# Kernel optimization log

Measured on AMD Instinct MI355X. Metric: run time of the kernel, lower is better.

Reference implementation:

```python
import jax, jax.numpy as jnp
import numpy as np
from jax import lax

N, C, RC, H, W = 2, 256, 32, 64, 64  # RC = C // 8


def conv1x1(x, w, b):
    # x: [n,c,h,w], w: [o,c], b: [o]
    return jnp.einsum('nchw,oc->nohw', x, w) + b[None, :, None, None]


def conv3x3(x, w, b):
    # x: [n,c,h,w], w: [o,i,3,3]
    y = lax.conv_general_dilated(x, w, window_strides=(1, 1), padding='SAME',
                                 dimension_numbers=('NCHW', 'OIHW', 'NCHW'))
    return y + b[None, :, None, None]


def setup_inputs() -> dict:
    key = jax.random.key(0)
    ks = jax.random.split(key, 16)
    p = lambda k, s: jax.random.normal(k, s, dtype=jnp.float32) * 0.02
    z = lambda o: jnp.zeros((o,), jnp.float32)
    return {
        'rgb_feat': jax.random.normal(ks[0], (N, C, H, W), jnp.float32),
        'chm_feat': jax.random.normal(ks[1], (N, C, H, W), jnp.float32),
        'rgb_q_w': p(ks[2], (RC, C)), 'rgb_q_b': z(RC),
        'rgb_k_w': p(ks[3], (RC, C)), 'rgb_k_b': z(RC),
        'rgb_v_w': p(ks[4], (C, C)), 'rgb_v_b': z(C),
        'depth_q_w': p(ks[5], (RC, C)), 'depth_q_b': z(RC),
        'depth_k_w': p(ks[6], (RC, C)), 'depth_k_b': z(RC),
        'depth_v_w': p(ks[7], (C, C)), 'depth_v_b': z(C),
        'gate_w': p(ks[8], (C, 2 * C)), 'gate_b': z(C),
        'fus1_w': p(ks[9], (2 * C, 2 * C)), 'fus1_b': z(2 * C),
        'fus2_w': p(ks[10], (2 * C, 2 * C, 3, 3)), 'fus2_b': z(2 * C),
        'fus3_w': p(ks[11], (C, 2 * C)), 'fus3_b': z(C),
        'skip_w': p(ks[12], (C, 2 * C)), 'skip_b': z(C),
    }


def reference(rgb_feat, chm_feat,
              rgb_q_w, rgb_q_b, rgb_k_w, rgb_k_b, rgb_v_w, rgb_v_b,
              depth_q_w, depth_q_b, depth_k_w, depth_k_b, depth_v_w, depth_v_b,
              gate_w, gate_b, fus1_w, fus1_b, fus2_w, fus2_b,
              fus3_w, fus3_b, skip_w, skip_b):
    n, c, h, w = rgb_feat.shape
    hw = h * w
    flat = lambda t: t.reshape(n, t.shape[1], hw)

    rq = flat(conv1x1(rgb_feat, rgb_q_w, rgb_q_b))       # [n,rc,hw]
    rk = flat(conv1x1(rgb_feat, rgb_k_w, rgb_k_b))       # [n,rc,hw]
    rv = flat(conv1x1(rgb_feat, rgb_v_w, rgb_v_b))       # [n,c,hw]
    dq = flat(conv1x1(chm_feat, depth_q_w, depth_q_b))   # [n,rc,hw]
    dk = flat(conv1x1(chm_feat, depth_k_w, depth_k_b))   # [n,rc,hw]
    dv = flat(conv1x1(chm_feat, depth_v_w, depth_v_b))   # [n,c,hw]

    # rgb branch attended with depth-derived attention
    rgb_attn = jax.nn.softmax(jnp.einsum('nri,nrj->nij', dq, dk), axis=-1)  # [n,hw,hw]
    br = jnp.einsum('nci,nij->ncj', rv, rgb_attn).reshape(rgb_feat.shape) + rgb_feat

    # depth branch attended with rgb-derived attention
    depth_attn = jax.nn.softmax(jnp.einsum('nri,nrj->nij', rq, rk), axis=-1)
    bd = jnp.einsum('nci,nij->ncj', dv, depth_attn).reshape(chm_feat.shape) + chm_feat

    cat = jnp.concatenate([br, bd], axis=1)              # [n,2c,h,w]
    g = jax.nn.sigmoid(conv1x1(cat, gate_w, gate_b))     # [n,c,h,w]
    c_fused = br * g + bd * (1.0 - g)
    d_fused = br * bd
    f = jnp.concatenate([c_fused, d_fused], axis=1)      # [n,2c,h,w]

    y = jax.nn.relu(conv1x1(f, fus1_w, fus1_b))
    y = jax.nn.relu(conv3x3(y, fus2_w, fus2_b))
    y = conv1x1(y, fus3_w, fus3_b)
    fused = y + conv1x1(f, skip_w, skip_b)
    return fused
```

## Files before the change

kernel.cpp:

```cpp
#include <hip/hip_runtime.h>
#include <stdint.h>


typedef __bf16 bf16_t;
typedef __bf16 bf16x8 __attribute__((ext_vector_type(8)));
typedef float f32x4 __attribute__((ext_vector_type(4)));

#define HW 4096
#define NB 2

__device__ inline f32x4 mfma_bf16(bf16x8 a, bf16x8 b, f32x4 c) {
    return __builtin_amdgcn_mfma_f32_16x16x32_bf16(a, b, c, 0, 0, 0);
}

#define MAXJOB 12
struct CvtJobs {
    const float* src[MAXJOB];
    bf16_t* dst[MAXJOB];
    int vend[MAXJOB];
    int rowlen[MAXJOB];
    int rowstride[MAXJOB];
    int rowoff[MAXJOB];
};

__global__ __launch_bounds__(256) void convert_batch_k(CvtJobs J, int totalvec) {
    int gv = blockIdx.x * 256 + threadIdx.x;
    if (gv >= totalvec) return;
    int j = 0;
    while (gv >= J.vend[j]) j++;
    int vbase = (j == 0) ? 0 : J.vend[j - 1];
    int e = (gv - vbase) * 8;
    const float* s = J.src[j] + e;
    float4 f0 = *(const float4*)s;
    float4 f1 = *(const float4*)(s + 4);
    bf16x8 o;
    o[0] = (bf16_t)f0.x; o[1] = (bf16_t)f0.y; o[2] = (bf16_t)f0.z; o[3] = (bf16_t)f0.w;
    o[4] = (bf16_t)f1.x; o[5] = (bf16_t)f1.y; o[6] = (bf16_t)f1.z; o[7] = (bf16_t)f1.w;
    int di = e;
    if (J.rowlen[j])
        di = (e / J.rowlen[j]) * J.rowstride[j] + J.rowoff[j] + (e % J.rowlen[j]);
    *(bf16x8*)(J.dst[j] + di) = o;
}

__global__ __launch_bounds__(256) void pack_bias_k(const float* qr, const float* kr,
                                                   const float* qd, const float* kd,
                                                   const float* sb, const float* fb,
                                                   float* BQK_R, float* BQK_D, float* BSUM) {
    int t = threadIdx.x;
    if (t < 32) {
        BQK_R[t] = qr[t]; BQK_R[32 + t] = kr[t];
        BQK_D[t] = qd[t]; BQK_D[32 + t] = kd[t];
    }
    BSUM[t] = sb[t] + fb[t];
}

__global__ __launch_bounds__(256) void reorder_fus2_k(const float* __restrict__ src,
                                                      bf16_t* __restrict__ dst) {
    int idx = blockIdx.x * 256 + threadIdx.x;
    if (idx >= 512 * 4608) return;
    int o = idx / 4608;
    int t = idx % 4608;
    int t9 = t / 512;
    int c  = t % 512;
    dst[idx] = (bf16_t)src[(size_t)o * 4608 + c * 9 + t9];
}

template <int EPI, bool OUT_BF16>
__global__ __launch_bounds__(256) void gemm_k(const bf16_t* __restrict__ A,
                                              const bf16_t* __restrict__ A2,
                                              const bf16_t* __restrict__ B,
                                              const float* __restrict__ bias,
                                              const float* __restrict__ bias2,
                                              void* __restrict__ outp,
                                              const void* __restrict__ aux,
                                              int M, int K, size_t strideB, size_t strideO) {
    __shared__ bf16_t Bt[64][72];
    const int t = threadIdx.x;
    const int mb = blockIdx.x, jb = blockIdx.y, n = blockIdx.z;
    const int w = t >> 6, lane = t & 63, quad = lane >> 4, l16 = lane & 15;

    const bf16_t* Au = (n >= 2) ? A2 : A;
    const float* biasu = (n >= 2) ? bias2 : bias;

    const bf16_t* Bb = B + (size_t)n * strideB + jb * 64;
    const int srow = t >> 2;
    const int scol = (t & 3) << 4;

    f32x4 zero = {0.f, 0.f, 0.f, 0.f};
    f32x4 acc[4] = {zero, zero, zero, zero};

    const bf16_t* Arow = Au + (size_t)(mb * 64 + w * 16 + l16) * K + quad * 8;

    for (int k0 = 0; k0 < K; k0 += 64) {
        const bf16_t* src = Bb + (size_t)(k0 + srow) * HW + scol;
        bf16x8 v0 = *(const bf16x8*)src;
        bf16x8 v1 = *(const bf16x8*)(src + 8);
        __syncthreads();
#pragma unroll
        for (int e = 0; e < 8; e++) Bt[scol + e][srow] = v0[e];
#pragma unroll
        for (int e = 0; e < 8; e++) Bt[scol + 8 + e][srow] = v1[e];
        __syncthreads();

        bf16x8 a0 = *(const bf16x8*)(Arow + k0);
        bf16x8 a1 = *(const bf16x8*)(Arow + k0 + 32);
#pragma unroll
        for (int ns = 0; ns < 4; ns++) {
            bf16x8 b0 = *(const bf16x8*)&Bt[ns * 16 + l16][quad * 8];
            bf16x8 b1 = *(const bf16x8*)&Bt[ns * 16 + l16][32 + quad * 8];
            acc[ns] = mfma_bf16(a0, b0, acc[ns]);
            acc[ns] = mfma_bf16(a1, b1, acc[ns]);
        }
    }

    if (EPI == 6) {
#pragma unroll
        for (int ns = 0; ns < 4; ns++) {
            int col = jb * 64 + ns * 16 + l16;
            union { bf16_t h[4]; unsigned long long u; } pk;
#pragma unroll
            for (int rr = 0; rr < 4; rr++) {
                int m = w * 16 + quad * 4 + rr;
                pk.h[rr] = (bf16_t)(acc[ns][rr] + biasu[m]);
            }
            *(unsigned long long*)((bf16_t*)outp +
                ((size_t)n * HW + col) * 64 + w * 16 + quad * 4) = pk.u;
        }
    } else if (EPI == 7) {
        const int m_base = mb * 64 + w * 16 + quad * 4;
#pragma unroll
        for (int ns = 0; ns < 4; ns++) {
            int col = jb * 64 + ns * 16 + l16;
            union { bf16_t h[4]; unsigned long long u; } pk;
#pragma unroll
            for (int rr = 0; rr < 4; rr++) {
                float v = acc[ns][rr] + biasu[m_base + rr];
                pk.h[rr] = (bf16_t)(v > 0.f ? v : 0.f);
            }
            *(unsigned long long*)((bf16_t*)outp +
                ((size_t)n * HW + col) * 512 + m_base) = pk.u;
        }
    } else if (EPI == 5) {
        const bf16_t* catp = (const bf16_t*)aux;
        bf16_t* f = (bf16_t*)outp;
#pragma unroll
        for (int ns = 0; ns < 4; ns++) {
#pragma unroll
            for (int rr = 0; rr < 4; rr++) {
                int m = mb * 64 + w * 16 + quad * 4 + rr;
                int col = jb * 64 + ns * 16 + l16;
                float v = acc[ns][rr] + biasu[m];
                float g = 1.f / (1.f + __expf(-v));
                size_t base = (size_t)n * 512 * HW + (size_t)m * HW + col;
                float br = (float)catp[base];
                float bd = (float)catp[base + (size_t)256 * HW];
                size_t ob = (size_t)n * 1024 * HW + (size_t)m * HW + col;
                f[ob] = (bf16_t)(br * g + bd * (1.f - g));
                f[ob + (size_t)256 * HW] = (bf16_t)(br * bd);
            }
        }
    } else {
#pragma unroll
        for (int ns = 0; ns < 4; ns++) {
#pragma unroll
            for (int rr = 0; rr < 4; rr++) {
                int m = mb * 64 + w * 16 + quad * 4 + rr;
                int col = jb * 64 + ns * 16 + l16;
                float v = acc[ns][rr] + biasu[m];
                if (EPI == 1) v = v > 0.f ? v : 0.f;
                else if (EPI == 3) v = v / ((const float*)aux)[n * HW + col];
                size_t oi = (size_t)n * strideO + (size_t)m * HW + col;
                if (OUT_BF16) ((bf16_t*)outp)[oi] = (bf16_t)v;
                else ((float*)outp)[oi] = v;
            }
        }
    }
}

__global__ __launch_bounds__(256) void conv3_k(const bf16_t* __restrict__ A,
                                               const bf16_t* __restrict__ Y1n,
                                               const float* __restrict__ bias,
                                               bf16_t* __restrict__ outp,
                                               size_t strideN) {
    __shared__ bf16_t kTn[198][72];
    const int t = threadIdx.x;
    const int mb = blockIdx.x, y = blockIdx.y, n = blockIdx.z;
    const int w = t >> 6, lane = t & 63, quad = lane >> 4, l16 = lane & 15;

    f32x4 zero = {0.f, 0.f, 0.f, 0.f};
    f32x4 acc[2][4];
#pragma unroll
    for (int i = 0; i < 2; i++)
#pragma unroll
        for (int j = 0; j < 4; j++) acc[i][j] = zero;

    const bf16_t* Yb = Y1n + (size_t)n * HW * 512;

    const bf16_t* Arow0 = A + (size_t)(mb * 128 + w * 32 + l16) * 4608 + quad * 8;
    const bf16_t* Arow1 = Arow0 + (size_t)16 * 4608;

    int pxs[7], seg[7], gidx[7];
    bool ok[7], act[7];
#pragma unroll
    for (int i = 0; i < 7; i++) {
        int slot = t + i * 256;
        act[i] = slot < 1584;
        int ps = act[i] ? (slot >> 3) : 0;
        pxs[i] = ps;
        seg[i] = slot & 7;
        int r = ps / 66, xm = ps % 66;
        int yy = y + r - 1, xx = xm - 1;
        ok[i] = act[i] && ((unsigned)yy < 64u) && ((unsigned)xx < 64u);
        gidx[i] = ok[i] ? (yy * 64 + xx) : 0;
    }

    for (int c0 = 0; c0 < 512; c0 += 64) {
        bf16x8 vals[7];
#pragma unroll
        for (int i = 0; i < 7; i++) {
            bf16x8 v;
            if (ok[i]) {
                v = *(const bf16x8*)(Yb + (size_t)gidx[i] * 512 + c0 + seg[i] * 8);
            } else {
#pragma unroll
                for (int e = 0; e < 8; e++) v[e] = (bf16_t)0.f;
            }
            vals[i] = v;
        }
        __syncthreads();
#pragma unroll
        for (int i = 0; i < 7; i++)
            if (act[i]) *(bf16x8*)&kTn[pxs[i]][seg[i] * 8] = vals[i];
        __syncthreads();

#pragma unroll
        for (int t9 = 0; t9 < 9; t9++) {
            const int dy = t9 / 3, dx = t9 % 3;
            const bf16_t* ap0 = Arow0 + t9 * 512 + c0;
            const bf16_t* ap1 = Arow1 + t9 * 512 + c0;
            bf16x8 a00 = *(const bf16x8*)(ap0);
            bf16x8 a01 = *(const bf16x8*)(ap0 + 32);
            bf16x8 a10 = *(const bf16x8*)(ap1);
            bf16x8 a11 = *(const bf16x8*)(ap1 + 32);
#pragma unroll
            for (int ns = 0; ns < 4; ns++) {
                int p = dy * 66 + ns * 16 + l16 + dx;
                bf16x8 b0 = *(const bf16x8*)&kTn[p][quad * 8];
                bf16x8 b1 = *(const bf16x8*)&kTn[p][32 + quad * 8];
                acc[0][ns] = mfma_bf16(a00, b0, acc[0][ns]);
                acc[0][ns] = mfma_bf16(a01, b1, acc[0][ns]);
                acc[1][ns] = mfma_bf16(a10, b0, acc[1][ns]);
                acc[1][ns] = mfma_bf16(a11, b1, acc[1][ns]);
            }
        }
    }

#pragma unroll
    for (int ms = 0; ms < 2; ms++) {
#pragma unroll
        for (int ns = 0; ns < 4; ns++) {
#pragma unroll
            for (int rr = 0; rr < 4; rr++) {
                int m = mb * 128 + w * 32 + ms * 16 + quad * 4 + rr;
                int x = ns * 16 + l16;
                float v = acc[ms][ns][rr] + bias[m];
                v = v > 0.f ? v : 0.f;
                outp[(size_t)n * strideN + (size_t)m * HW + y * 64 + x] = (bf16_t)v;
            }
        }
    }
}

__global__ __launch_bounds__(256) void rowsum_k(const bf16_t* __restrict__ QKT,
                                                float* __restrict__ Z) {
    __shared__ float Zp[2][32];
    const int t = threadIdx.x, ib = blockIdx.x, k = blockIdx.y;
    const int w = t >> 6, lane = t & 63, quad = lane >> 4, l16 = lane & 15;
    const int is = w & 1, jh = w >> 1;
    const int qs = k ^ 2;
    const bf16_t* Q = QKT + (size_t)qs * HW * 64;

    bf16x8 a = *(const bf16x8*)(Q + (size_t)(ib * 32 + is * 16 + l16) * 64 + quad * 8);
    float zacc[4] = {0.f, 0.f, 0.f, 0.f};
    f32x4 zero = {0.f, 0.f, 0.f, 0.f};

    for (int jt = jh * 32; jt < jh * 32 + 32; jt++) {
#pragma unroll
        for (int ns = 0; ns < 4; ns++) {
            bf16x8 b = *(const bf16x8*)(Q + (size_t)(jt * 64 + ns * 16 + l16) * 64 + 32 + quad * 8);
            f32x4 s = mfma_bf16(a, b, zero);
#pragma unroll
            for (int rr = 0; rr < 4; rr++) zacc[rr] += __expf(s[rr]);
        }
    }

#pragma unroll
    for (int rr = 0; rr < 4; rr++) {
        for (int mask = 1; mask < 16; mask <<= 1)
            zacc[rr] += __shfl_xor(zacc[rr], mask, 64);
    }
    if (l16 == 0) {
#pragma unroll
        for (int rr = 0; rr < 4; rr++)
            Zp[jh][is * 16 + quad * 4 + rr] = zacc[rr];
    }
    __syncthreads();
    if (t < 32)
        Z[(size_t)k * HW + ib * 32 + t] = Zp[0][t] + Zp[1][t];
}

__global__ __launch_bounds__(256) void attn3_k(const bf16_t* __restrict__ QKT,
                                               const bf16_t* __restrict__ V,
                                               const float* __restrict__ rgb_feat,
                                               const float* __restrict__ chm_feat,
                                               bf16_t* __restrict__ CAT) {
    __shared__ bf16_t PT[2][64][72];
    const int t = threadIdx.x, cb = blockIdx.x, jb = blockIdx.y, z = blockIdx.z;
    const int w = t >> 6, lane = t & 63, quad = lane >> 4, l16 = lane & 15;
    const int qs = z ^ 2, n = z & 1;

    const bf16_t* Q = QKT + (size_t)qs * HW * 64;

    bf16x8 bS[4];
#pragma unroll
    for (int ns = 0; ns < 4; ns++)
        bS[ns] = *(const bf16x8*)(Q + (size_t)(jb * 64 + ns * 16 + l16) * 64 + 32 + quad * 8);

    f32x4 zero = {0.f, 0.f, 0.f, 0.f};
    f32x4 acc[2][4];
#pragma unroll
    for (int i = 0; i < 2; i++)
#pragma unroll
        for (int j = 0; j < 4; j++) acc[i][j] = zero;

    const bf16_t* Vr0 = V + ((size_t)z * 256 + cb * 128 + w * 16 + l16) * HW + quad * 8;
    const bf16_t* Vr1 = Vr0 + (size_t)64 * HW;

    for (int it = 0; it < 64; it++) {
        const int p = it & 1;
        bf16x8 aS = *(const bf16x8*)(Q + (size_t)(it * 64 + w * 16 + l16) * 64 + quad * 8);
        bf16x8 aV[2][2];
        aV[0][0] = *(const bf16x8*)(Vr0 + it * 64);
        aV[0][1] = *(const bf16x8*)(Vr0 + it * 64 + 32);
        aV[1][0] = *(const bf16x8*)(Vr1 + it * 64);
        aV[1][1] = *(const bf16x8*)(Vr1 + it * 64 + 32);

#pragma unroll
        for (int ns = 0; ns < 4; ns++) {
            f32x4 s = mfma_bf16(aS, bS[ns], zero);
            union { bf16_t h[4]; unsigned long long u; } pk;
#pragma unroll
            for (int rr = 0; rr < 4; rr++) pk.h[rr] = (bf16_t)__expf(s[rr]);
            *(unsigned long long*)&PT[p][ns * 16 + l16][w * 16 + quad * 4] = pk.u;
        }
        __syncthreads();

#pragma unroll
        for (int ns = 0; ns < 4; ns++) {
            bf16x8 b0 = *(const bf16x8*)&PT[p][ns * 16 + l16][quad * 8];
            bf16x8 b1 = *(const bf16x8*)&PT[p][ns * 16 + l16][32 + quad * 8];
#pragma unroll
            for (int ct = 0; ct < 2; ct++) {
                acc[ct][ns] = mfma_bf16(aV[ct][0], b0, acc[ct][ns]);
                acc[ct][ns] = mfma_bf16(aV[ct][1], b1, acc[ct][ns]);
            }
        }
    }

    const float* feat = ((z < 2) ? rgb_feat : chm_feat) + (size_t)n * 256 * HW;
    bf16_t* outp = CAT + (size_t)n * 512 * HW + (size_t)(z < 2 ? 0 : 256) * HW;
#pragma unroll
    for (int ct = 0; ct < 2; ct++) {
#pragma unroll
        for (int ns = 0; ns < 4; ns++) {
#pragma unroll
            for (int rr = 0; rr < 4; rr++) {
                int c = cb * 128 + ct * 64 + w * 16 + quad * 4 + rr;
                int col = jb * 64 + ns * 16 + l16;
                float v = acc[ct][ns][rr] + feat[(size_t)c * HW + col];
                outp[(size_t)c * HW + col] = (bf16_t)v;
            }
        }
    }
}

extern "C" void kernel_launch(void* const* d_in, const int* in_sizes, int n_in,
                              void* d_out, int out_size, void* d_ws, size_t ws_size,
                              hipStream_t stream) {
    (void)in_sizes; (void)n_in; (void)out_size; (void)ws_size;

    const float* rgb_feat  = (const float*)d_in[0];
    const float* chm_feat  = (const float*)d_in[1];
    const float* rgb_q_w   = (const float*)d_in[2];
    const float* rgb_q_b   = (const float*)d_in[3];
    const float* rgb_k_w   = (const float*)d_in[4];
    const float* rgb_k_b   = (const float*)d_in[5];
    const float* rgb_v_w   = (const float*)d_in[6];
    const float* rgb_v_b   = (const float*)d_in[7];
    const float* depth_q_w = (const float*)d_in[8];
    const float* depth_q_b = (const float*)d_in[9];
    const float* depth_k_w = (const float*)d_in[10];
    const float* depth_k_b = (const float*)d_in[11];
    const float* depth_v_w = (const float*)d_in[12];
    const float* depth_v_b = (const float*)d_in[13];
    const float* gate_w    = (const float*)d_in[14];
    const float* gate_b    = (const float*)d_in[15];
    const float* fus1_w    = (const float*)d_in[16];
    const float* fus1_b    = (const float*)d_in[17];
    const float* fus2_w    = (const float*)d_in[18];
    const float* fus2_b    = (const float*)d_in[19];
    const float* fus3_w    = (const float*)d_in[20];
    const float* fus3_b    = (const float*)d_in[21];
    const float* skip_w    = (const float*)d_in[22];
    const float* skip_b    = (const float*)d_in[23];

    char* ws = (char*)d_ws;
    size_t off = 0;
    auto alloc = [&](size_t bytes) -> char* {
        char* p = ws + off;
        off += (bytes + 255) & ~(size_t)255;
        return p;
    };

    bf16_t* WQK_R = (bf16_t*)alloc(64 * 256 * 2);
    bf16_t* WQK_D = (bf16_t*)alloc(64 * 256 * 2);
    bf16_t* WV_R  = (bf16_t*)alloc(256 * 256 * 2);
    bf16_t* WV_D  = (bf16_t*)alloc(256 * 256 * 2);
    bf16_t* WGATE = (bf16_t*)alloc(256 * 512 * 2);
    bf16_t* WFUS1 = (bf16_t*)alloc(512 * 512 * 2);
    bf16_t* WFUS2 = (bf16_t*)alloc(512 * 4608 * 2);
    bf16_t* WCAT  = (bf16_t*)alloc(256 * 1024 * 2);
    float*  BQK_R = (float*)alloc(64 * 4);
    float*  BQK_D = (float*)alloc(64 * 4);
    float*  BSUM  = (float*)alloc(256 * 4);
    bf16_t* XB    = (bf16_t*)alloc((size_t)4 * 256 * HW * 2);
    bf16_t* QKT   = (bf16_t*)alloc((size_t)4 * HW * 64 * 2);
    float*  ZBUF  = (float*)alloc((size_t)4 * HW * 4);
    bf16_t* V4    = (bf16_t*)alloc((size_t)4 * 256 * HW * 2);
    bf16_t* CAT   = (bf16_t*)alloc((size_t)NB * 512 * HW * 2);
    bf16_t* FY    = (bf16_t*)alloc((size_t)NB * 1024 * HW * 2);
    bf16_t* Y1    = (bf16_t*)alloc((size_t)NB * HW * 512 * 2);

    bf16_t* XR = XB;
    bf16_t* XC = XB + (size_t)2 * 256 * HW;

    CvtJobs J;
    int cum = 0, nj = 0;
    auto addjob = [&](const float* s, bf16_t* d, int cnt, int rl, int rs, int ro) {
        J.src[nj] = s; J.dst[nj] = d; cum += cnt / 8; J.vend[nj] = cum;
        J.rowlen[nj] = rl; J.rowstride[nj] = rs; J.rowoff[nj] = ro; nj++;
    };
    addjob(rgb_feat, XR, NB * 256 * HW, 0, 0, 0);
    addjob(chm_feat, XC, NB * 256 * HW, 0, 0, 0);
    addjob(rgb_q_w, WQK_R, 32 * 256, 0, 0, 0);
    addjob(rgb_k_w, WQK_R + 32 * 256, 32 * 256, 0, 0, 0);
    addjob(depth_q_w, WQK_D, 32 * 256, 0, 0, 0);
    addjob(depth_k_w, WQK_D + 32 * 256, 32 * 256, 0, 0, 0);
    addjob(rgb_v_w, WV_R, 256 * 256, 0, 0, 0);
    addjob(depth_v_w, WV_D, 256 * 256, 0, 0, 0);
    addjob(gate_w, WGATE, 256 * 512, 0, 0, 0);
    addjob(fus1_w, WFUS1, 512 * 512, 0, 0, 0);
    addjob(skip_w, WCAT, 256 * 512, 512, 1024, 0);
    addjob(fus3_w, WCAT, 256 * 512, 512, 1024, 512);
    int totalvec = cum;
    convert_batch_k<<<dim3((totalvec + 255) / 256), 256, 0, stream>>>(J, totalvec);
    reorder_fus2_k<<<dim3(512 * 4608 / 256), 256, 0, stream>>>(fus2_w, WFUS2);
    pack_bias_k<<<dim3(1), 256, 0, stream>>>(rgb_q_b, rgb_k_b, depth_q_b, depth_k_b,
                                             skip_b, fus3_b, BQK_R, BQK_D, BSUM);

    gemm_k<6, true><<<dim3(1, 64, 4), 256, 0, stream>>>(
        WQK_R, WQK_D, XB, BQK_R, BQK_D, QKT, nullptr, 64, 256, (size_t)256 * HW, 0);

    rowsum_k<<<dim3(128, 4), 256, 0, stream>>>(QKT, ZBUF);

    gemm_k<3, true><<<dim3(4, 64, 4), 256, 0, stream>>>(
        WV_R, WV_D, XB, rgb_v_b, depth_v_b, V4, ZBUF, 256, 256, (size_t)256 * HW, (size_t)256 * HW);

    attn3_k<<<dim3(2, 64, 4), 256, 0, stream>>>(QKT, V4, rgb_feat, chm_feat, CAT);

    gemm_k<5, true><<<dim3(4, 64, NB), 256, 0, stream>>>(
        WGATE, WGATE, CAT, gate_b, gate_b, FY, CAT, 256, 512, (size_t)512 * HW, 0);

    gemm_k<7, true><<<dim3(8, 64, NB), 256, 0, stream>>>(
        WFUS1, WFUS1, FY, fus1_b, fus1_b, Y1, nullptr, 512, 512, (size_t)1024 * HW, 0);

    conv3_k<<<dim3(4, 64, NB), 256, 0, stream>>>(WFUS2, Y1, fus2_b,
                                                 FY + (size_t)512 * HW, (size_t)1024 * HW);

    gemm_k<0, false><<<dim3(4, 64, NB), 256, 0, stream>>>(
        WCAT, WCAT, FY, BSUM, BSUM, d_out, nullptr, 256, 1024, (size_t)1024 * HW, (size_t)256 * HW);
}
```

Baseline: 389.0 us.

## Warp-specialize attention kernel into score producers and PV consumers

The attention kernel is rewritten so each 512-thread block covers all 256 channels for one column tile. Four producer waves compute exp(QK) tiles into double-buffered shared memory one iteration ahead, while four consumer waves prefetch V and run the PV MFMAs. This removes the duplicate score computation the old channel-split grid did per block and overlaps exp with MFMA work. The trade-off is that half the grid is gone (256 blocks of 512 threads instead of 512 of 256), consumer register pressure is higher, and producer waves sit idle in the epilogue.

Result: no change. 391.8 us (+0.7%).

```diff
diff --git a/kernel.cpp b/kernel.cpp
--- a/kernel.cpp
+++ b/kernel.cpp
@@ -309,76 +309,112 @@
         Z[(size_t)k * HW + ib * 32 + t] = Zp[0][t] + Zp[1][t];
 }
 
-__global__ __launch_bounds__(256) void attn3_k(const bf16_t* __restrict__ QKT,
+__global__ __launch_bounds__(512) void attn4_k(const bf16_t* __restrict__ QKT,
                                                const bf16_t* __restrict__ V,
                                                const float* __restrict__ rgb_feat,
                                                const float* __restrict__ chm_feat,
                                                bf16_t* __restrict__ CAT) {
     __shared__ bf16_t PT[2][64][72];
-    const int t = threadIdx.x, cb = blockIdx.x, jb = blockIdx.y, z = blockIdx.z;
+    const int t = threadIdx.x, jb = blockIdx.x, z = blockIdx.y;
     const int w = t >> 6, lane = t & 63, quad = lane >> 4, l16 = lane & 15;
     const int qs = z ^ 2, n = z & 1;
+    const bool prod = (w < 4);
+    const int pw = w, cw = w - 4;
 
     const bf16_t* Q = QKT + (size_t)qs * HW * 64;
+    f32x4 zero = {0.f, 0.f, 0.f, 0.f};
 
     bf16x8 bS[4];
-#pragma unroll
-    for (int ns = 0; ns < 4; ns++)
-        bS[ns] = *(const bf16x8*)(Q + (size_t)(jb * 64 + ns * 16 + l16) * 64 + 32 + quad * 8);
-
-    f32x4 zero = {0.f, 0.f, 0.f, 0.f};
-    f32x4 acc[2][4];
-#pragma unroll
-    for (int i = 0; i < 2; i++)
+    if (prod) {
+#pragma unroll
+        for (int ns = 0; ns < 4; ns++)
+            bS[ns] = *(const bf16x8*)(Q + (size_t)(jb * 64 + ns * 16 + l16) * 64 + 32 + quad * 8);
+    }
+    f32x4 acc[4][4];
+#pragma unroll
+    for (int i = 0; i < 4; i++)
 #pragma unroll
         for (int j = 0; j < 4; j++) acc[i][j] = zero;
-
-    const bf16_t* Vr0 = V + ((size_t)z * 256 + cb * 128 + w * 16 + l16) * HW + quad * 8;
-    const bf16_t* Vr1 = Vr0 + (size_t)64 * HW;
+    const bf16_t* Vp = V + ((size_t)z * 256 + cw * 16 + l16) * HW + quad * 8;
+    bf16x8 aV[4][2], aVn[4][2];
+
+    if (prod) {
+        bf16x8 aS = *(const bf16x8*)(Q + (size_t)(pw * 16 + l16) * 64 + quad * 8);
+#pragma unroll
+        for (int ns = 0; ns < 4; ns++) {
+            f32x4 s = mfma_bf16(aS, bS[ns], zero);
+            union { bf16_t h[4]; unsigned long long u; } pk;
+#pragma unroll
+            for (int rr = 0; rr < 4; rr++) pk.h[rr] = (bf16_t)__expf(s[rr]);
+            *(unsigned long long*)&PT[0][ns * 16 + l16][pw * 16 + quad * 4] = pk.u;
+        }
+    } else {
+#pragma unroll
+        for (int ct = 0; ct < 4; ct++) {
+            aV[ct][0] = *(const bf16x8*)(Vp + (size_t)ct * 64 * HW);
+            aV[ct][1] = *(const bf16x8*)(Vp + (size_t)ct * 64 * HW + 32);
+        }
+    }
+    __syncthreads();
 
     for (int it = 0; it < 64; it++) {
         const int p = it & 1;
-        bf16x8 aS = *(const bf16x8*)(Q + (size_t)(it * 64 + w * 16 + l16) * 64 + quad * 8);
-        bf16x8 aV[2][2];
-        aV[0][0] = *(const bf16x8*)(Vr0 + it * 64);
-        aV[0][1] = *(const bf16x8*)(Vr0 + it * 64 + 32);
-        aV[1][0] = *(const bf16x8*)(Vr1 + it * 64);
-        aV[1][1] = *(const bf16x8*)(Vr1 + it * 64 + 32);
-
-#pragma unroll
-        for (int ns = 0; ns < 4; ns++) {
-            f32x4 s = mfma_bf16(aS, bS[ns], zero);
-            union { bf16_t h[4]; unsigned long long u; } pk;
-#pragma unroll
-            for (int rr = 0; rr < 4; rr++) pk.h[rr] = (bf16_t)__expf(s[rr]);
-            *(unsigned long long*)&PT[p][ns * 16 + l16][w * 16 + quad * 4] = pk.u;
+        if (prod) {
+            if (it < 63) {
+                bf16x8 aS = *(const bf16x8*)(Q + (size_t)((it + 1) * 64 + pw * 16 + l16) * 64 + quad * 8);
+#pragma unroll
+                for (int ns = 0; ns < 4; ns++) {
+                    f32x4 s = mfma_bf16(aS, bS[ns], zero);
+                    union { bf16_t h[4]; unsigned long long u; } pk;
+#pragma unroll
+                    for (int rr = 0; rr < 4; rr++) pk.h[rr] = (bf16_t)__expf(s[rr]);
+                    *(unsigned long long*)&PT[p ^ 1][ns * 16 + l16][pw * 16 + quad * 4] = pk.u;
+                }
+            }
+        } else {
+            if (it < 63) {
+                const bf16_t* vp = Vp + (it + 1) * 64;
+#pragma unroll
+                for (int ct = 0; ct < 4; ct++) {
+                    aVn[ct][0] = *(const bf16x8*)(vp + (size_t)ct * 64 * HW);
+                    aVn[ct][1] = *(const bf16x8*)(vp + (size_t)ct * 64 * HW + 32);
+                }
+            }
+#pragma unroll
+            for (int ns = 0; ns < 4; ns++) {
+                bf16x8 b0 = *(const bf16x8*)&PT[p][ns * 16 + l16][quad * 8];
+                bf16x8 b1 = *(const bf16x8*)&PT[p][ns * 16 + l16][32 + quad * 8];
+#pragma unroll
+                for (int ct = 0; ct < 4; ct++) {
+                    acc[ct][ns] = mfma_bf16(aV[ct][0], b0, acc[ct][ns]);
+                    acc[ct][ns] = mfma_bf16(aV[ct][1], b1, acc[ct][ns]);
+                }
+            }
         }
         __syncthreads();
-
-#pragma unroll
-        for (int ns = 0; ns < 4; ns++) {
-            bf16x8 b0 = *(const bf16x8*)&PT[p][ns * 16 + l16][quad * 8];
-            bf16x8 b1 = *(const bf16x8*)&PT[p][ns * 16 + l16][32 + quad * 8];
-#pragma unroll
-            for (int ct = 0; ct < 2; ct++) {
-                acc[ct][ns] = mfma_bf16(aV[ct][0], b0, acc[ct][ns]);
-                acc[ct][ns] = mfma_bf16(aV[ct][1], b1, acc[ct][ns]);
-            }
-        }
-    }
-
-    const float* feat = ((z < 2) ? rgb_feat : chm_feat) + (size_t)n * 256 * HW;
-    bf16_t* outp = CAT + (size_t)n * 512 * HW + (size_t)(z < 2 ? 0 : 256) * HW;
-#pragma unroll
-    for (int ct = 0; ct < 2; ct++) {
-#pragma unroll
-        for (int ns = 0; ns < 4; ns++) {
-#pragma unroll
-            for (int rr = 0; rr < 4; rr++) {
-                int c = cb * 128 + ct * 64 + w * 16 + quad * 4 + rr;
-                int col = jb * 64 + ns * 16 + l16;
-                float v = acc[ct][ns][rr] + feat[(size_t)c * HW + col];
-                outp[(size_t)c * HW + col] = (bf16_t)v;
+        if (!prod && it < 63) {
+#pragma unroll
+            for (int ct = 0; ct < 4; ct++) {
+                aV[ct][0] = aVn[ct][0];
+                aV[ct][1] = aVn[ct][1];
+            }
+        }
+    }
+
+    if (!prod) {
+        const float* feat = ((z < 2) ? rgb_feat : chm_feat) + (size_t)n * 256 * HW;
+        bf16_t* outp = CAT + (size_t)n * 512 * HW + (size_t)(z < 2 ? 0 : 256) * HW;
+#pragma unroll
+        for (int ct = 0; ct < 4; ct++) {
+#pragma unroll
+            for (int ns = 0; ns < 4; ns++) {
+#pragma unroll
+                for (int rr = 0; rr < 4; rr++) {
+                    int c = ct * 64 + cw * 16 + quad * 4 + rr;
+                    int col = jb * 64 + ns * 16 + l16;
+                    float v = acc[ct][ns][rr] + feat[(size_t)c * HW + col];
+                    outp[(size_t)c * HW + col] = (bf16_t)v;
+                }
             }
         }
     }
@@ -476,7 +512,7 @@
     gemm_k<3, true><<<dim3(4, 64, 4), 256, 0, stream>>>(
         WV_R, WV_D, XB, rgb_v_b, depth_v_b, V4, ZBUF, 256, 256, (size_t)256 * HW, (size_t)256 * HW);
 
-    attn3_k<<<dim3(2, 64, 4), 256, 0, stream>>>(QKT, V4, rgb_feat, chm_feat, CAT);
+    attn4_k<<<dim3(64, 4), 512, 0, stream>>>(QKT, V4, rgb_feat, chm_feat, CAT);
 
     gemm_k<5, true><<<dim3(4, 64, NB), 256, 0, stream>>>(
         WGATE, WGATE, CAT, gate_b, gate_b, FY, CAT, 256, 512, (size_t)512 * HW, 0);
```

## Keep attention probabilities in registers using 16x16x16 MFMA, removing LDS round-trip

Applied to the files above, without the earlier changes.

Rewrites the attention-times-V kernel so each block covers all 256 channels for 32 query columns. The exp'd scores come out of the QK MFMA in exactly the B-operand layout of the 16x16x16 bf16 MFMA, so they feed the PV product directly. This removes the shared-memory transpose and the per-iteration __syncthreads. The trade-offs are that scores are no longer recomputed per channel half, the PV MFMA is a smaller K=16 instruction issuing twice as often, V loads are narrower 8-byte reads, and the grid changes to 4x128 blocks.

New measurement: 594.3 us. 52.8% more time.

```diff
diff --git a/kernel.cpp b/kernel.cpp
--- a/kernel.cpp
+++ b/kernel.cpp
@@ -4,6 +4,8 @@
 
 typedef __bf16 bf16_t;
 typedef __bf16 bf16x8 __attribute__((ext_vector_type(8)));
+typedef __bf16 bf16x4 __attribute__((ext_vector_type(4)));
+typedef short short4_t __attribute__((ext_vector_type(4)));
 typedef float f32x4 __attribute__((ext_vector_type(4)));
 
 #define HW 4096
@@ -11,6 +13,12 @@
 
 __device__ inline f32x4 mfma_bf16(bf16x8 a, bf16x8 b, f32x4 c) {
     return __builtin_amdgcn_mfma_f32_16x16x32_bf16(a, b, c, 0, 0, 0);
+}
+
+__device__ inline f32x4 mfma16_bf16(bf16x4 a, bf16x4 b, f32x4 c) {
+    union { bf16x4 h; short4_t s; } ua, ub;
+    ua.h = a; ub.h = b;
+    return __builtin_amdgcn_mfma_f32_16x16x16bf16_1k(ua.s, ub.s, c, 0, 0, 0);
 }
 
 #define MAXJOB 12
@@ -309,75 +317,63 @@
         Z[(size_t)k * HW + ib * 32 + t] = Zp[0][t] + Zp[1][t];
 }
 
-__global__ __launch_bounds__(256) void attn3_k(const bf16_t* __restrict__ QKT,
+__global__ __launch_bounds__(256) void attn5_k(const bf16_t* __restrict__ QKT,
                                                const bf16_t* __restrict__ V,
                                                const float* __restrict__ rgb_feat,
                                                const float* __restrict__ chm_feat,
                                                bf16_t* __restrict__ CAT) {
-    __shared__ bf16_t PT[2][64][72];
-    const int t = threadIdx.x, cb = blockIdx.x, jb = blockIdx.y, z = blockIdx.z;
+    const int t = threadIdx.x, z = blockIdx.x, jb = blockIdx.y;
     const int w = t >> 6, lane = t & 63, quad = lane >> 4, l16 = lane & 15;
     const int qs = z ^ 2, n = z & 1;
 
     const bf16_t* Q = QKT + (size_t)qs * HW * 64;
-
-    bf16x8 bS[4];
-#pragma unroll
-    for (int ns = 0; ns < 4; ns++)
-        bS[ns] = *(const bf16x8*)(Q + (size_t)(jb * 64 + ns * 16 + l16) * 64 + 32 + quad * 8);
-
     f32x4 zero = {0.f, 0.f, 0.f, 0.f};
-    f32x4 acc[2][4];
-#pragma unroll
-    for (int i = 0; i < 2; i++)
-#pragma unroll
-        for (int j = 0; j < 4; j++) acc[i][j] = zero;
-
-    const bf16_t* Vr0 = V + ((size_t)z * 256 + cb * 128 + w * 16 + l16) * HW + quad * 8;
-    const bf16_t* Vr1 = Vr0 + (size_t)64 * HW;
-
-    for (int it = 0; it < 64; it++) {
-        const int p = it & 1;
-        bf16x8 aS = *(const bf16x8*)(Q + (size_t)(it * 64 + w * 16 + l16) * 64 + quad * 8);
-        bf16x8 aV[2][2];
-        aV[0][0] = *(const bf16x8*)(Vr0 + it * 64);
-        aV[0][1] = *(const bf16x8*)(Vr0 + it * 64 + 32);
-        aV[1][0] = *(const bf16x8*)(Vr1 + it * 64);
-        aV[1][1] = *(const bf16x8*)(Vr1 + it * 64 + 32);
-
-#pragma unroll
-        for (int ns = 0; ns < 4; ns++) {
-            f32x4 s = mfma_bf16(aS, bS[ns], zero);
-            union { bf16_t h[4]; unsigned long long u; } pk;
-#pragma unroll
-            for (int rr = 0; rr < 4; rr++) pk.h[rr] = (bf16_t)__expf(s[rr]);
-            *(unsigned long long*)&PT[p][ns * 16 + l16][w * 16 + quad * 4] = pk.u;
-        }
-        __syncthreads();
-
-#pragma unroll
-        for (int ns = 0; ns < 4; ns++) {
-            bf16x8 b0 = *(const bf16x8*)&PT[p][ns * 16 + l16][quad * 8];
-            bf16x8 b1 = *(const bf16x8*)&PT[p][ns * 16 + l16][32 + quad * 8];
-#pragma unroll
-            for (int ct = 0; ct < 2; ct++) {
-                acc[ct][ns] = mfma_bf16(aV[ct][0], b0, acc[ct][ns]);
-                acc[ct][ns] = mfma_bf16(aV[ct][1], b1, acc[ct][ns]);
-            }
+
+    bf16x8 bS[2];
+#pragma unroll
+    for (int js = 0; js < 2; js++)
+        bS[js] = *(const bf16x8*)(Q + (size_t)(jb * 32 + js * 16 + l16) * 64 + 32 + quad * 8);
+
+    f32x4 acc[4][2];
+#pragma unroll
+    for (int i = 0; i < 4; i++)
+#pragma unroll
+        for (int j = 0; j < 2; j++) acc[i][j] = zero;
+
+    const bf16_t* Vb = V + ((size_t)z * 256 + w * 64 + l16) * HW + quad * 4;
+
+#pragma unroll 2
+    for (int it = 0; it < 256; it++) {
+        const int i0 = it * 16;
+        bf16x8 aS = *(const bf16x8*)(Q + (size_t)(i0 + l16) * 64 + quad * 8);
+        bf16x4 aV[4];
+#pragma unroll
+        for (int ct = 0; ct < 4; ct++)
+            aV[ct] = *(const bf16x4*)(Vb + (size_t)(ct * 16) * HW + i0);
+
+#pragma unroll
+        for (int js = 0; js < 2; js++) {
+            f32x4 s = mfma_bf16(aS, bS[js], zero);
+            bf16x4 p;
+#pragma unroll
+            for (int rr = 0; rr < 4; rr++) p[rr] = (bf16_t)__expf(s[rr]);
+#pragma unroll
+            for (int ct = 0; ct < 4; ct++)
+                acc[ct][js] = mfma16_bf16(aV[ct], p, acc[ct][js]);
         }
     }
 
     const float* feat = ((z < 2) ? rgb_feat : chm_feat) + (size_t)n * 256 * HW;
     bf16_t* outp = CAT + (size_t)n * 512 * HW + (size_t)(z < 2 ? 0 : 256) * HW;
 #pragma unroll
-    for (int ct = 0; ct < 2; ct++) {
-#pragma unroll
-        for (int ns = 0; ns < 4; ns++) {
-#pragma unroll
-            for (int rr = 0; rr < 4; rr++) {
-                int c = cb * 128 + ct * 64 + w * 16 + quad * 4 + rr;
-                int col = jb * 64 + ns * 16 + l16;
-                float v = acc[ct][ns][rr] + feat[(size_t)c * HW + col];
+    for (int ct = 0; ct < 4; ct++) {
+#pragma unroll
+        for (int js = 0; js < 2; js++) {
+#pragma unroll
+            for (int rr = 0; rr < 4; rr++) {
+                int c = w * 64 + ct * 16 + quad * 4 + rr;
+                int col = jb * 32 + js * 16 + l16;
+                float v = acc[ct][js][rr] + feat[(size_t)c * HW + col];
                 outp[(size_t)c * HW + col] = (bf16_t)v;
             }
         }
@@ -476,7 +472,7 @@
     gemm_k<3, true><<<dim3(4, 64, 4), 256, 0, stream>>>(
         WV_R, WV_D, XB, rgb_v_b, depth_v_b, V4, ZBUF, 256, 256, (size_t)256 * HW, (size_t)256 * HW);
 
-    attn3_k<<<dim3(2, 64, 4), 256, 0, stream>>>(QKT, V4, rgb_feat, chm_feat, CAT);
+    attn5_k<<<dim3(4, 128), 256, 0, stream>>>(QKT, V4, rgb_feat, chm_feat, CAT);
 
     gemm_k<5, true><<<dim3(4, 64, NB), 256, 0, stream>>>(
         WGATE, WGATE, CAT, gate_b, gate_b, FY, CAT, 256, 512, (size_t)512 * HW, 0);
```

## Halve attention and conv3x3 pixel tiles to double grid size; merge prep kernels

Applied to the files above, without the earlier changes.

The attention kernel now processes 32 query columns per block instead of 64. The 3x3 conv now processes half-rows of 32 pixels. Each of these launches twice as many blocks, to raise occupancy and spread work across more CUs. The three preprocessing kernels (weight conversion, fus2 reorder, bias packing) are merged into one launch to cut launch overhead. In exchange, the smaller tiles make the attention kernel recompute exp scores against more V reloads, and the conv reloads weights and halo data more often per output.

After: 510.0 us. 31.1% more time.

```diff
diff --git a/kernel.cpp b/kernel.cpp
--- a/kernel.cpp
+++ b/kernel.cpp
@@ -23,46 +23,45 @@
     int rowoff[MAXJOB];
 };
 
-__global__ __launch_bounds__(256) void convert_batch_k(CvtJobs J, int totalvec) {
-    int gv = blockIdx.x * 256 + threadIdx.x;
-    if (gv >= totalvec) return;
-    int j = 0;
-    while (gv >= J.vend[j]) j++;
-    int vbase = (j == 0) ? 0 : J.vend[j - 1];
-    int e = (gv - vbase) * 8;
-    const float* s = J.src[j] + e;
-    float4 f0 = *(const float4*)s;
-    float4 f1 = *(const float4*)(s + 4);
-    bf16x8 o;
-    o[0] = (bf16_t)f0.x; o[1] = (bf16_t)f0.y; o[2] = (bf16_t)f0.z; o[3] = (bf16_t)f0.w;
-    o[4] = (bf16_t)f1.x; o[5] = (bf16_t)f1.y; o[6] = (bf16_t)f1.z; o[7] = (bf16_t)f1.w;
-    int di = e;
-    if (J.rowlen[j])
-        di = (e / J.rowlen[j]) * J.rowstride[j] + J.rowoff[j] + (e % J.rowlen[j]);
-    *(bf16x8*)(J.dst[j] + di) = o;
-}
-
-__global__ __launch_bounds__(256) void pack_bias_k(const float* qr, const float* kr,
-                                                   const float* qd, const float* kd,
-                                                   const float* sb, const float* fb,
-                                                   float* BQK_R, float* BQK_D, float* BSUM) {
-    int t = threadIdx.x;
-    if (t < 32) {
-        BQK_R[t] = qr[t]; BQK_R[32 + t] = kr[t];
-        BQK_D[t] = qd[t]; BQK_D[32 + t] = kd[t];
-    }
-    BSUM[t] = sb[t] + fb[t];
-}
-
-__global__ __launch_bounds__(256) void reorder_fus2_k(const float* __restrict__ src,
-                                                      bf16_t* __restrict__ dst) {
-    int idx = blockIdx.x * 256 + threadIdx.x;
-    if (idx >= 512 * 4608) return;
-    int o = idx / 4608;
-    int t = idx % 4608;
-    int t9 = t / 512;
-    int c  = t % 512;
-    dst[idx] = (bf16_t)src[(size_t)o * 4608 + c * 9 + t9];
+__global__ __launch_bounds__(256) void prep_k(CvtJobs J, int totalvec, int cvtBlocks,
+                                              const float* __restrict__ fus2src,
+                                              bf16_t* __restrict__ fus2dst,
+                                              const float* qr, const float* kr,
+                                              const float* qd, const float* kd,
+                                              const float* sb, const float* fb,
+                                              float* BQK_R, float* BQK_D, float* BSUM) {
+    const int b = blockIdx.x, t = threadIdx.x;
+    if (b < cvtBlocks) {
+        int gv = b * 256 + t;
+        if (gv >= totalvec) return;
+        int j = 0;
+        while (gv >= J.vend[j]) j++;
+        int vbase = (j == 0) ? 0 : J.vend[j - 1];
+        int e = (gv - vbase) * 8;
+        const float* s = J.src[j] + e;
+        float4 f0 = *(const float4*)s;
+        float4 f1 = *(const float4*)(s + 4);
+        bf16x8 o;
+        o[0] = (bf16_t)f0.x; o[1] = (bf16_t)f0.y; o[2] = (bf16_t)f0.z; o[3] = (bf16_t)f0.w;
+        o[4] = (bf16_t)f1.x; o[5] = (bf16_t)f1.y; o[6] = (bf16_t)f1.z; o[7] = (bf16_t)f1.w;
+        int di = e;
+        if (J.rowlen[j])
+            di = (e / J.rowlen[j]) * J.rowstride[j] + J.rowoff[j] + (e % J.rowlen[j]);
+        *(bf16x8*)(J.dst[j] + di) = o;
+    } else if (b < cvtBlocks + 9216) {
+        int idx = (b - cvtBlocks) * 256 + t;
+        int o = idx / 4608;
+        int tt = idx % 4608;
+        int t9 = tt / 512;
+        int c  = tt % 512;
+        fus2dst[idx] = (bf16_t)fus2src[(size_t)o * 4608 + c * 9 + t9];
+    } else {
+        if (t < 32) {
+            BQK_R[t] = qr[t]; BQK_R[32 + t] = kr[t];
+            BQK_D[t] = qd[t]; BQK_D[32 + t] = kd[t];
+        }
+        BSUM[t] = sb[t] + fb[t];
+    }
 }
 
 template <int EPI, bool OUT_BF16>
@@ -182,42 +181,43 @@
                                                const float* __restrict__ bias,
                                                bf16_t* __restrict__ outp,
                                                size_t strideN) {
-    __shared__ bf16_t kTn[198][72];
+    __shared__ bf16_t kTn[102][72];
     const int t = threadIdx.x;
-    const int mb = blockIdx.x, y = blockIdx.y, n = blockIdx.z;
+    const int mb = blockIdx.x, pb = blockIdx.y, n = blockIdx.z;
     const int w = t >> 6, lane = t & 63, quad = lane >> 4, l16 = lane & 15;
+    const int y = pb >> 1, x0t = (pb & 1) * 32;
 
     f32x4 zero = {0.f, 0.f, 0.f, 0.f};
-    f32x4 acc[2][4];
+    f32x4 acc[2][2];
 #pragma unroll
     for (int i = 0; i < 2; i++)
 #pragma unroll
-        for (int j = 0; j < 4; j++) acc[i][j] = zero;
+        for (int j = 0; j < 2; j++) acc[i][j] = zero;
 
     const bf16_t* Yb = Y1n + (size_t)n * HW * 512;
 
     const bf16_t* Arow0 = A + (size_t)(mb * 128 + w * 32 + l16) * 4608 + quad * 8;
     const bf16_t* Arow1 = Arow0 + (size_t)16 * 4608;
 
-    int pxs[7], seg[7], gidx[7];
-    bool ok[7], act[7];
-#pragma unroll
-    for (int i = 0; i < 7; i++) {
+    int pxs[4], seg[4], gidx[4];
+    bool ok[4], act[4];
+#pragma unroll
+    for (int i = 0; i < 4; i++) {
         int slot = t + i * 256;
-        act[i] = slot < 1584;
+        act[i] = slot < 816;
         int ps = act[i] ? (slot >> 3) : 0;
         pxs[i] = ps;
         seg[i] = slot & 7;
-        int r = ps / 66, xm = ps % 66;
-        int yy = y + r - 1, xx = xm - 1;
+        int r = ps / 34, xm = ps % 34;
+        int yy = y + r - 1, xx = x0t + xm - 1;
         ok[i] = act[i] && ((unsigned)yy < 64u) && ((unsigned)xx < 64u);
         gidx[i] = ok[i] ? (yy * 64 + xx) : 0;
     }
 
     for (int c0 = 0; c0 < 512; c0 += 64) {
-        bf16x8 vals[7];
-#pragma unroll
-        for (int i = 0; i < 7; i++) {
+        bf16x8 vals[4];
+#pragma unroll
+        for (int i = 0; i < 4; i++) {
             bf16x8 v;
             if (ok[i]) {
                 v = *(const bf16x8*)(Yb + (size_t)gidx[i] * 512 + c0 + seg[i] * 8);
@@ -229,7 +229,7 @@
         }
         __syncthreads();
 #pragma unroll
-        for (int i = 0; i < 7; i++)
+        for (int i = 0; i < 4; i++)
             if (act[i]) *(bf16x8*)&kTn[pxs[i]][seg[i] * 8] = vals[i];
         __syncthreads();
 
@@ -243,8 +243,8 @@
             bf16x8 a10 = *(const bf16x8*)(ap1);
             bf16x8 a11 = *(const bf16x8*)(ap1 + 32);
 #pragma unroll
-            for (int ns = 0; ns < 4; ns++) {
-                int p = dy * 66 + ns * 16 + l16 + dx;
+            for (int ns = 0; ns < 2; ns++) {
+                int p = dy * 34 + ns * 16 + l16 + dx;
                 bf16x8 b0 = *(const bf16x8*)&kTn[p][quad * 8];
                 bf16x8 b1 = *(const bf16x8*)&kTn[p][32 + quad * 8];
                 acc[0][ns] = mfma_bf16(a00, b0, acc[0][ns]);
@@ -258,11 +258,11 @@
 #pragma unroll
     for (int ms = 0; ms < 2; ms++) {
 #pragma unroll
-        for (int ns = 0; ns < 4; ns++) {
+        for (int ns = 0; ns < 2; ns++) {
 #pragma unroll
             for (int rr = 0; rr < 4; rr++) {
                 int m = mb * 128 + w * 32 + ms * 16 + quad * 4 + rr;
-                int x = ns * 16 + l16;
+                int x = x0t + ns * 16 + l16;
                 float v = acc[ms][ns][rr] + bias[m];
                 v = v > 0.f ? v : 0.f;
                 outp[(size_t)n * strideN + (size_t)m * HW + y * 64 + x] = (bf16_t)v;
@@ -309,29 +309,29 @@
         Z[(size_t)k * HW + ib * 32 + t] = Zp[0][t] + Zp[1][t];
 }
 
-__global__ __launch_bounds__(256) void attn3_k(const bf16_t* __restrict__ QKT,
+__global__ __launch_bounds__(256) void attn6_k(const bf16_t* __restrict__ QKT,
                                                const bf16_t* __restrict__ V,
                                                const float* __restrict__ rgb_feat,
                                                const float* __restrict__ chm_feat,
                                                bf16_t* __restrict__ CAT) {
-    __shared__ bf16_t PT[2][64][72];
+    __shared__ bf16_t PT[2][32][72];
     const int t = threadIdx.x, cb = blockIdx.x, jb = blockIdx.y, z = blockIdx.z;
     const int w = t >> 6, lane = t & 63, quad = lane >> 4, l16 = lane & 15;
     const int qs = z ^ 2, n = z & 1;
 
     const bf16_t* Q = QKT + (size_t)qs * HW * 64;
 
-    bf16x8 bS[4];
-#pragma unroll
-    for (int ns = 0; ns < 4; ns++)
-        bS[ns] = *(const bf16x8*)(Q + (size_t)(jb * 64 + ns * 16 + l16) * 64 + 32 + quad * 8);
+    bf16x8 bS[2];
+#pragma unroll
+    for (int js = 0; js < 2; js++)
+        bS[js] = *(const bf16x8*)(Q + (size_t)(jb * 32 + js * 16 + l16) * 64 + 32 + quad * 8);
 
     f32x4 zero = {0.f, 0.f, 0.f, 0.f};
-    f32x4 acc[2][4];
+    f32x4 acc[2][2];
 #pragma unroll
     for (int i = 0; i < 2; i++)
 #pragma unroll
-        for (int j = 0; j < 4; j++) acc[i][j] = zero;
+        for (int j = 0; j < 2; j++) acc[i][j] = zero;
 
     const bf16_t* Vr0 = V + ((size_t)z * 256 + cb * 128 + w * 16 + l16) * HW + quad * 8;
     const bf16_t* Vr1 = Vr0 + (size_t)64 * HW;
@@ -346,23 +346,23 @@
         aV[1][1] = *(const bf16x8*)(Vr1 + it * 64 + 32);
 
 #pragma unroll
-        for (int ns = 0; ns < 4; ns++) {
-            f32x4 s = mfma_bf16(aS, bS[ns], zero);
+        for (int js = 0; js < 2; js++) {
+            f32x4 s = mfma_bf16(aS, bS[js], zero);
             union { bf16_t h[4]; unsigned long long u; } pk;
 #pragma unroll
             for (int rr = 0; rr < 4; rr++) pk.h[rr] = (bf16_t)__expf(s[rr]);
-            *(unsigned long long*)&PT[p][ns * 16 + l16][w * 16 + quad * 4] = pk.u;
+            *(unsigned long long*)&PT[p][js * 16 + l16][w * 16 + quad * 4] = pk.u;
         }
         __syncthreads();
 
 #pragma unroll
-        for (int ns = 0; ns < 4; ns++) {
-            bf16x8 b0 = *(const bf16x8*)&PT[p][ns * 16 + l16][quad * 8];
-            bf16x8 b1 = *(const bf16x8*)&PT[p][ns * 16 + l16][32 + quad * 8];
+        for (int js = 0; js < 2; js++) {
+            bf16x8 b0 = *(const bf16x8*)&PT[p][js * 16 + l16][quad * 8];
+            bf16x8 b1 = *(const bf16x8*)&PT[p][js * 16 + l16][32 + quad * 8];
 #pragma unroll
             for (int ct = 0; ct < 2; ct++) {
-                acc[ct][ns] = mfma_bf16(aV[ct][0], b0, acc[ct][ns]);
-                acc[ct][ns] = mfma_bf16(aV[ct][1], b1, acc[ct][ns]);
+                acc[ct][js] = mfma_bf16(aV[ct][0], b0, acc[ct][js]);
+                acc[ct][js] = mfma_bf16(aV[ct][1], b1, acc[ct][js]);
             }
         }
     }
@@ -372,12 +372,12 @@
 #pragma unroll
     for (int ct = 0; ct < 2; ct++) {
 #pragma unroll
-        for (int ns = 0; ns < 4; ns++) {
+        for (int js = 0; js < 2; js++) {
 #pragma unroll
             for (int rr = 0; rr < 4; rr++) {
                 int c = cb * 128 + ct * 64 + w * 16 + quad * 4 + rr;
-                int col = jb * 64 + ns * 16 + l16;
-                float v = acc[ct][ns][rr] + feat[(size_t)c * HW + col];
+                int col = jb * 32 + js * 16 + l16;
+                float v = acc[ct][js][rr] + feat[(size_t)c * HW + col];
                 outp[(size_t)c * HW + col] = (bf16_t)v;
             }
         }
@@ -463,10 +463,11 @@
     addjob(skip_w, WCAT, 256 * 512, 512, 1024, 0);
     addjob(fus3_w, WCAT, 256 * 512, 512, 1024, 512);
     int totalvec = cum;
-    convert_batch_k<<<dim3((totalvec + 255) / 256), 256, 0, stream>>>(J, totalvec);
-    reorder_fus2_k<<<dim3(512 * 4608 / 256), 256, 0, stream>>>(fus2_w, WFUS2);
-    pack_bias_k<<<dim3(1), 256, 0, stream>>>(rgb_q_b, rgb_k_b, depth_q_b, depth_k_b,
-                                             skip_b, fus3_b, BQK_R, BQK_D, BSUM);
+    int cvtBlocks = (totalvec + 255) / 256;
+    prep_k<<<dim3(cvtBlocks + 9216 + 1), 256, 0, stream>>>(
+        J, totalvec, cvtBlocks, fus2_w, WFUS2,
+        rgb_q_b, rgb_k_b, depth_q_b, depth_k_b, skip_b, fus3_b,
+        BQK_R, BQK_D, BSUM);
 
     gemm_k<6, true><<<dim3(1, 64, 4), 256, 0, stream>>>(
         WQK_R, WQK_D, XB, BQK_R, BQK_D, QKT, nullptr, 64, 256, (size_t)256 * HW, 0);
@@ -476,7 +477,7 @@
     gemm_k<3, true><<<dim3(4, 64, 4), 256, 0, stream>>>(
         WV_R, WV_D, XB, rgb_v_b, depth_v_b, V4, ZBUF, 256, 256, (size_t)256 * HW, (size_t)256 * HW);
 
-    attn3_k<<<dim3(2, 64, 4), 256, 0, stream>>>(QKT, V4, rgb_feat, chm_feat, CAT);
+    attn6_k<<<dim3(2, 128, 4), 256, 0, stream>>>(QKT, V4, rgb_feat, chm_feat, CAT);
 
     gemm_k<5, true><<<dim3(4, 64, NB), 256, 0, stream>>>(
         WGATE, WGATE, CAT, gate_b, gate_b, FY, CAT, 256, 512, (size_t)512 * HW, 0);
@@ -484,8 +485,8 @@
     gemm_k<7, true><<<dim3(8, 64, NB), 256, 0, stream>>>(
         WFUS1, WFUS1, FY, fus1_b, fus1_b, Y1, nullptr, 512, 512, (size_t)1024 * HW, 0);
 
-    conv3_k<<<dim3(4, 64, NB), 256, 0, stream>>>(WFUS2, Y1, fus2_b,
-                                                 FY + (size_t)512 * HW, (size_t)1024 * HW);
+    conv3_k<<<dim3(4, 128, NB), 256, 0, stream>>>(WFUS2, Y1, fus2_b,
+                                                  FY + (size_t)512 * HW, (size_t)1024 * HW);
 
     gemm_k<0, false><<<dim3(4, 64, NB), 256, 0, stream>>>(
         WCAT, WCAT, FY, BSUM, BSUM, d_out, nullptr, 256, 1024, (size_t)1024 * HW, (size_t)256 * HW);
```
